# Kernel optimization log

Measured on AMD Instinct MI355X. Metric: run time of the kernel, lower is better.

Reference implementation:

```python
import jax, jax.numpy as jnp
import numpy as np

B, S, D, HU = 64, 512, 256, 1024
W_SCALE = 0.01  # flax nn.initializers.normal() default stddev


def setup_inputs() -> dict:
    key = jax.random.key(0)
    ks = jax.random.split(key, 13)
    inp = {
        "inputs": jax.random.normal(ks[0], (B, S, D), dtype=jnp.float32),
        "H0": jax.random.normal(ks[1], (B, HU), dtype=jnp.float32),
        "C0": jax.random.normal(ks[2], (B, HU), dtype=jnp.float32),
        "Wxi": jax.random.normal(ks[3], (D, HU), dtype=jnp.float32) * W_SCALE,
        "Whi": jax.random.normal(ks[4], (HU, HU), dtype=jnp.float32) * W_SCALE,
        "bi": jnp.zeros((HU,), dtype=jnp.float32),
        "Wxf": jax.random.normal(ks[5], (D, HU), dtype=jnp.float32) * W_SCALE,
        "Whf": jax.random.normal(ks[6], (HU, HU), dtype=jnp.float32) * W_SCALE,
        "bf": jnp.zeros((HU,), dtype=jnp.float32),
        "Wxo": jax.random.normal(ks[7], (D, HU), dtype=jnp.float32) * W_SCALE,
        "Who": jax.random.normal(ks[8], (HU, HU), dtype=jnp.float32) * W_SCALE,
        "bo": jnp.zeros((HU,), dtype=jnp.float32),
        "Wxc": jax.random.normal(ks[9], (D, HU), dtype=jnp.float32) * W_SCALE,
        "Whc": jax.random.normal(ks[10], (HU, HU), dtype=jnp.float32) * W_SCALE,
        "bc": jnp.zeros((HU,), dtype=jnp.float32),
        "Wd": jax.random.normal(ks[11], (HU, 1), dtype=jnp.float32) * W_SCALE,
        "bd": jnp.zeros((1,), dtype=jnp.float32),
    }
    return inp


def _lstm_forward(inputs, H0, C0, Wxi, Whi, bi, Wxf, Whf, bf,
                  Wxo, Who, bo, Wxc, Whc, bc, Wd, bd):
    Hn = H0.shape[1]
    # Pack the 4 gate projections so the input GEMM is done once for all timesteps.
    Wx = jnp.concatenate([Wxi, Wxf, Wxo, Wxc], axis=1)  # (D, 4H)
    Wh = jnp.concatenate([Whi, Whf, Who, Whc], axis=1)  # (H, 4H)
    b = jnp.concatenate([bi, bf, bo, bc])                # (4H,)
    xg = jnp.einsum('bsd,dk->bsk', inputs, Wx) + b       # (B, S, 4H)

    def step(carry, xg_t):
        H, C = carry
        g = xg_t + H @ Wh                                # (B, 4H)
        i = jax.nn.sigmoid(g[:, :Hn])
        f = jax.nn.sigmoid(g[:, Hn:2 * Hn])
        o = jax.nn.sigmoid(g[:, 2 * Hn:3 * Hn])
        c_tilde = jnp.tanh(g[:, 3 * Hn:])
        C = f * C + i * c_tilde
        H = o * jnp.tanh(C)
        return (H, C), H

    (Hf, Cf), Hs = jax.lax.scan(step, (H0, C0), jnp.swapaxes(xg, 0, 1))
    outputs = jnp.swapaxes(Hs, 0, 1)                     # (B, S, H)
    pred = outputs @ Wd + bd                             # (B, S, 1)
    return pred, (Hf, Cf)


def reference(inputs, H0, C0, Wxi, Whi, bi, Wxf, Whf, bf,
              Wxo, Who, bo, Wxc, Whc, bc, Wd, bd):
    return _lstm_forward(inputs, H0, C0, Wxi, Whi, bi, Wxf, Whf, bf,
                         Wxo, Who, bo, Wxc, Whc, bc, Wd, bd)
```

## Files before the change

### kernel.cpp

```cpp
#include <hip/hip_runtime.h>


#define NB   128
#define SEQ  512
#define BATCH 64
#define DIM  256
#define HU   1024
#define ROWU 1032

typedef unsigned short u16;
typedef unsigned int   u32;
typedef unsigned long long u64;
typedef __attribute__((ext_vector_type(8))) short  short8;
typedef __attribute__((ext_vector_type(4))) float  f32x4;

typedef const __attribute__((address_space(1))) void* gptr_t;
typedef __attribute__((address_space(3))) void*       lptr_t;

__device__ __forceinline__ u16 f2bf(float x) {
  u32 u = __float_as_uint(x);
  u32 r = (u + 0x7FFFu + ((u >> 16) & 1u)) >> 16;
  return (u16)r;
}
__device__ __forceinline__ float sigf(float x)  { return 1.0f / (1.0f + __expf(-x)); }
__device__ __forceinline__ float tanhfast(float x) { return 1.0f - 2.0f / (1.0f + __expf(2.0f * x)); }
__device__ __forceinline__ short8 cv8(uint4 v) {
  union { uint4 d; short8 s; } u; u.d = v; return u.s;
}


__global__ void k_prep(const float* __restrict__ H0, u16* __restrict__ Hbuf0,
                       u32* __restrict__ flags) {
  int i = blockIdx.x * 256 + threadIdx.x;
  if (i < 2048) flags[i] = 0u;
  Hbuf0[i] = f2bf(H0[i]);
}

__global__ void k_xconv(const float* __restrict__ in, u16* __restrict__ out) {
  int i = blockIdx.x * 256 + threadIdx.x;
  float4 v = ((const float4*)in)[i];
  ushort4 o;
  o.x = f2bf(v.x); o.y = f2bf(v.y); o.z = f2bf(v.z); o.w = f2bf(v.w);
  ((ushort4*)out)[i] = o;
}

__global__ void k_pack(const float* __restrict__ Wxi, const float* __restrict__ Whi,
                       const float* __restrict__ Wxf, const float* __restrict__ Whf,
                       const float* __restrict__ Wxo, const float* __restrict__ Who,
                       const float* __restrict__ Wxc, const float* __restrict__ Whc,
                       u16* __restrict__ Wpack) {
  int tid  = blockIdx.x * 256 + threadIdx.x;
  int lane = tid & 63;
  int kc   = (tid >> 6) % 40;
  int nt   = ((tid >> 6) / 40) & 7;
  int bj   = (tid >> 6) / 320;
  int c    = nt * 16 + (lane & 15);
  int gate = (c >> 3) & 3;
  int h    = bj * 32 + (c >> 5) * 8 + (c & 7);
  const float* Wx = (gate == 0) ? Wxi : (gate == 1) ? Wxf : (gate == 2) ? Wxo : Wxc;
  const float* Wh = (gate == 0) ? Whi : (gate == 1) ? Whf : (gate == 2) ? Who : Whc;
  int kbase = kc * 32 + ((lane >> 4) << 3);
  u16 tmp[8];
#pragma unroll
  for (int e = 0; e < 8; e++) {
    int k = kbase + e;
    float v = (k < DIM) ? Wx[k * HU + h] : Wh[(k - DIM) * HU + h];
    tmp[e] = f2bf(v);
  }
  *(uint4*)(Wpack + (size_t)tid * 8) = *(uint4*)tmp;
}

__global__ void k_predsum(const float* __restrict__ part, const float* __restrict__ bd,
                          float* __restrict__ pred) {
  int i = blockIdx.x * 256 + threadIdx.x;
  int b = i & 63, t = i >> 6;
  float s = bd[0];
  const float* p0 = part + (size_t)t * NB * 64 + b;
#pragma unroll 8
  for (int jj = 0; jj < NB; jj++) s += p0[jj * 64];
  pred[b * SEQ + t] = s;
}


struct MainParams {
  const u16* __restrict__ xbf;
  const u16* __restrict__ Wpack;
  u16* __restrict__ Hbuf;
  const float* __restrict__ C0;
  const float* __restrict__ Wd;
  const float* __restrict__ bi;
  const float* __restrict__ bfg;
  const float* __restrict__ bo;
  const float* __restrict__ bc;
  float* __restrict__ ppart;
  float* __restrict__ Hf;
  float* __restrict__ Cf;
  u32* __restrict__ flags;
};

__global__ __launch_bounds__(256, 1) void lstm_main(MainParams p) {
  __shared__ __align__(16) u16 Hsm[16 * ROWU];

  const int tid  = threadIdx.x;
  const int wv   = tid >> 6, lane = tid & 63;
  const int bj   = blockIdx.x >> 2, bb = blockIdx.x & 3;
  const int q    = lane >> 4;
  const int q8   = q * 8;
  const int m16  = lane & 15;
  const int hl   = lane & 7;
  const bool hiH = (lane & 8) != 0;

  const int hglob = bj * 32 + wv * 8 + hl;
  const int row0  = 16 * bb;

  short8 wx[8][2], wh[32][2];
  {
    const u16* wbase = p.Wpack + ((size_t)bj * 8 + 2 * wv) * (40 * 512) + lane * 8;
#pragma unroll
    for (int kc = 0; kc < 8; kc++)
#pragma unroll
      for (int ntl = 0; ntl < 2; ntl++)
        wx[kc][ntl] = *(const short8*)(wbase + ((size_t)ntl * 40 + kc) * 512);
#pragma unroll
    for (int kc = 0; kc < 32; kc++)
#pragma unroll
      for (int ntl = 0; ntl < 2; ntl++)
        wh[kc][ntl] = *(const short8*)(wbase + ((size_t)ntl * 40 + 8 + kc) * 512);
  }

  const float bI = p.bi[hglob],  bF = p.bfg[hglob];
  const float bO = p.bo[hglob],  bC = p.bc[hglob];
  const float wdv = p.Wd[hglob];
  float Cst[4], Hst[4];
#pragma unroll
  for (int r = 0; r < 4; r++) {
    Cst[r] = p.C0[(row0 + q * 4 + r) * HU + hglob];
    Hst[r] = 0.f;
  }

  const u16* Aw = Hsm + m16 * ROWU + q8;

  uint4 ax[8];
#pragma unroll
  for (int kc = 0; kc < 8; kc++)
    ax[kc] = *(const uint4*)(p.xbf + ((size_t)((row0 + m16) * SEQ + 0)) * DIM
                             + kc * 32 + q8);

#pragma unroll 1
  for (int t = 0; t < SEQ; t++) {
    const int rb = t & 1;
    const u16* Hr = p.Hbuf + (size_t)rb * (BATCH * HU);
    u16*       Hw = p.Hbuf + (size_t)(rb ^ 1) * (BATCH * HU);

#pragma unroll
    for (int i = 0; i < 8; i++) {
      int s = wv * 8 + i, row = s >> 1, half = s & 1;
      const u16* g = Hr + (size_t)(row0 + row) * HU + half * 512 + lane * 8;
      __builtin_amdgcn_global_load_lds((gptr_t)(const void*)g,
          (lptr_t)(void*)(Hsm + row * ROWU + half * 512), 16, 0, 17);
    }

    f32x4 acc[2][4];
#pragma unroll
    for (int ntl = 0; ntl < 2; ntl++)
#pragma unroll
      for (int c = 0; c < 4; c++) acc[ntl][c] = (f32x4){0.f, 0.f, 0.f, 0.f};
#pragma unroll
    for (int kc = 0; kc < 8; kc++) {
      short8 af = cv8(ax[kc]);
      acc[0][kc & 3] = __builtin_amdgcn_mfma_f32_16x16x32_bf16(af, wx[kc][0], acc[0][kc & 3], 0, 0, 0);
      acc[1][kc & 3] = __builtin_amdgcn_mfma_f32_16x16x32_bf16(af, wx[kc][1], acc[1][kc & 3], 0, 0, 0);
    }

    __syncthreads();

    {
      const int tn = (t + 1 < SEQ) ? t + 1 : t;
#pragma unroll
      for (int kc = 0; kc < 8; kc++)
        ax[kc] = *(const uint4*)(p.xbf + ((size_t)((row0 + m16) * SEQ + tn)) * DIM
                                 + kc * 32 + q8);
    }

#pragma unroll
    for (int kc = 0; kc < 32; kc++) {
      short8 af = *(const short8*)(Aw + kc * 32);
      acc[0][kc & 3] = __builtin_amdgcn_mfma_f32_16x16x32_bf16(af, wh[kc][0], acc[0][kc & 3], 0, 0, 0);
      acc[1][kc & 3] = __builtin_amdgcn_mfma_f32_16x16x32_bf16(af, wh[kc][1], acc[1][kc & 3], 0, 0, 0);
    }

    f32x4 g01 = (acc[0][0] + acc[0][1]) + (acc[0][2] + acc[0][3]);
    f32x4 g23 = (acc[1][0] + acc[1][1]) + (acc[1][2] + acc[1][3]);

    float pr[4];
#pragma unroll
    for (int r = 0; r < 4; r++) {
      float u0 = g01[r], u1 = g23[r];
      float v0 = __shfl_xor(u0, 8);
      float v1 = __shfl_xor(u1, 8);
      float gi = hiH ? v0 : u0, gf = hiH ? u0 : v0;
      float go = hiH ? v1 : u1, gc = hiH ? u1 : v1;
      float iv = sigf(gi + bI), fv = sigf(gf + bF);
      float ov = sigf(go + bO), ct = tanhfast(gc + bC);
      Cst[r] = fv * Cst[r] + iv * ct;
      Hst[r] = ov * tanhfast(Cst[r]);
      pr[r]  = Hst[r] * wdv;
    }

    if (!hiH) {
#pragma unroll
      for (int r = 0; r < 4; r++)
        __hip_atomic_store(Hw + (size_t)(row0 + q * 4 + r) * HU + hglob,
                           f2bf(Hst[r]), __ATOMIC_RELAXED, __HIP_MEMORY_SCOPE_AGENT);
    }

#pragma unroll
    for (int r = 0; r < 4; r++) {
      pr[r] += __shfl_xor(pr[r], 1);
      pr[r] += __shfl_xor(pr[r], 2);
      pr[r] += __shfl_xor(pr[r], 4);
    }
    if (m16 == 0) {
      float4 st = {pr[0], pr[1], pr[2], pr[3]};
      *(float4*)(p.ppart + (((size_t)t * 32 + bj) * 4 + wv) * 64 + row0 + q * 4) = st;
    }

    __syncthreads();
    if (tid == 0)
      __hip_atomic_store(p.flags + (bb * 32 + bj) * 16, (u32)(t + 1),
                         __ATOMIC_RELAXED, __HIP_MEMORY_SCOPE_AGENT);
    if (tid < 32) {
      const u32* f = p.flags + (bb * 32 + tid) * 16;
      while (__hip_atomic_load(f, __ATOMIC_RELAXED, __HIP_MEMORY_SCOPE_AGENT) < (u32)(t + 1))
        __builtin_amdgcn_s_sleep(1);
    }
    __syncthreads();
  }

  if (!hiH) {
#pragma unroll
    for (int r = 0; r < 4; r++) {
      int row = row0 + q * 4 + r;
      p.Hf[row * HU + hglob] = Hst[r];
      p.Cf[row * HU + hglob] = Cst[r];
    }
  }
}


extern "C" void kernel_launch(void* const* d_in, const int* in_sizes, int n_in,
                              void* d_out, int out_size, void* d_ws, size_t ws_size,
                              hipStream_t stream) {
  const float* inputs = (const float*)d_in[0];
  const float* H0  = (const float*)d_in[1];
  const float* C0  = (const float*)d_in[2];
  const float* Wxi = (const float*)d_in[3];
  const float* Whi = (const float*)d_in[4];
  const float* bi  = (const float*)d_in[5];
  const float* Wxf = (const float*)d_in[6];
  const float* Whf = (const float*)d_in[7];
  const float* bf_ = (const float*)d_in[8];
  const float* Wxo = (const float*)d_in[9];
  const float* Who = (const float*)d_in[10];
  const float* bo  = (const float*)d_in[11];
  const float* Wxc = (const float*)d_in[12];
  const float* Whc = (const float*)d_in[13];
  const float* bc  = (const float*)d_in[14];
  const float* Wd  = (const float*)d_in[15];
  const float* bd  = (const float*)d_in[16];

  char* ws = (char*)d_ws;
  u32*   flags = (u32*)ws;
  u16*   Wpack = (u16*)(ws + 8192);
  u16*   xbf   = (u16*)(ws + 8192 + 10485760);
  u16*   Hbuf  = (u16*)(ws + 8192 + 10485760 + 16777216);
  float* ppart = (float*)(ws + 8192 + 10485760 + 16777216 + 262144);

  float* pred = (float*)d_out;
  float* Hf   = pred + BATCH * SEQ;
  float* Cf   = Hf + BATCH * HU;

  k_prep<<<256, 256, 0, stream>>>(H0, Hbuf, flags);
  k_xconv<<<8192, 256, 0, stream>>>(inputs, xbf);
  k_pack<<<2560, 256, 0, stream>>>(Wxi, Whi, Wxf, Whf, Wxo, Who, Wxc, Whc, Wpack);

  MainParams prm{xbf, Wpack, Hbuf, C0, Wd, bi, bf_, bo, bc, ppart, Hf, Cf, flags};
  lstm_main<<<dim3(NB), dim3(256), 0, stream>>>(prm);

  k_predsum<<<128, 256, 0, stream>>>(ppart, bd, pred);
}
```

Measured before the change: 2.338 ms.

## Replace block barriers with per-wave flags and stream H directly from global

Drops the two __syncthreads-based block-level handshakes. Each wave now publishes its own progress flag after storing its slice of H, and all 64 lanes poll the 128 wave flags for their batch group before reading H. The recurrent A operand is read with relaxed atomic 64-bit global loads straight into registers, double-buffered across groups of four k-chunks, so the LDS staging copy goes away. The new H values are packed through a small LDS buffer so each wave writes contiguous 16-byte rows. This is meant to shorten the per-step critical path, at the cost of more flag polling traffic and correctness that depends on waitcnt ordering of the relaxed stores.

```diff
diff --git a/kernel.cpp b/kernel.cpp
--- a/kernel.cpp
+++ b/kernel.cpp
@@ -6,7 +6,6 @@
 #define BATCH 64
 #define DIM  256
 #define HU   1024
-#define ROWU 1032
 
 typedef unsigned short u16;
 typedef unsigned int   u32;
@@ -14,8 +13,8 @@
 typedef __attribute__((ext_vector_type(8))) short  short8;
 typedef __attribute__((ext_vector_type(4))) float  f32x4;
 
-typedef const __attribute__((address_space(1))) void* gptr_t;
-typedef __attribute__((address_space(3))) void*       lptr_t;
+#define AL_RLX(p)    __hip_atomic_load((p),  __ATOMIC_RELAXED, __HIP_MEMORY_SCOPE_AGENT)
+#define AS_RLX(p, v) __hip_atomic_store((p), (v), __ATOMIC_RELAXED, __HIP_MEMORY_SCOPE_AGENT)
 
 __device__ __forceinline__ u16 f2bf(float x) {
   u32 u = __float_as_uint(x);
@@ -27,12 +26,15 @@
 __device__ __forceinline__ short8 cv8(uint4 v) {
   union { uint4 d; short8 s; } u; u.d = v; return u.s;
 }
+__device__ __forceinline__ short8 mk8(u64 lo, u64 hi) {
+  union { u64 d[2]; short8 s; } u; u.d[0] = lo; u.d[1] = hi; return u.s;
+}
 
 
 __global__ void k_prep(const float* __restrict__ H0, u16* __restrict__ Hbuf0,
                        u32* __restrict__ flags) {
   int i = blockIdx.x * 256 + threadIdx.x;
-  if (i < 2048) flags[i] = 0u;
+  if (i < 8192) flags[i] = 0u;
   Hbuf0[i] = f2bf(H0[i]);
 }
 
@@ -99,7 +101,7 @@
 };
 
 __global__ __launch_bounds__(256, 1) void lstm_main(MainParams p) {
-  __shared__ __align__(16) u16 Hsm[16 * ROWU];
+  __shared__ u16 Hpub[4 * 128];
 
   const int tid  = threadIdx.x;
   const int wv   = tid >> 6, lane = tid & 63;
@@ -138,13 +140,14 @@
     Hst[r] = 0.f;
   }
 
-  const u16* Aw = Hsm + m16 * ROWU + q8;
-
   uint4 ax[8];
 #pragma unroll
   for (int kc = 0; kc < 8; kc++)
     ax[kc] = *(const uint4*)(p.xbf + ((size_t)((row0 + m16) * SEQ + 0)) * DIM
                              + kc * 32 + q8);
+
+  const u32* fbase = p.flags + (size_t)bb * 128 * 16;
+  u32* myflag = p.flags + ((size_t)(bb * 32 + bj) * 4 + wv) * 16;
 
 #pragma unroll 1
   for (int t = 0; t < SEQ; t++) {
@@ -152,12 +155,26 @@
     const u16* Hr = p.Hbuf + (size_t)rb * (BATCH * HU);
     u16*       Hw = p.Hbuf + (size_t)(rb ^ 1) * (BATCH * HU);
 
-#pragma unroll
-    for (int i = 0; i < 8; i++) {
-      int s = wv * 8 + i, row = s >> 1, half = s & 1;
-      const u16* g = Hr + (size_t)(row0 + row) * HU + half * 512 + lane * 8;
-      __builtin_amdgcn_global_load_lds((gptr_t)(const void*)g,
-          (lptr_t)(void*)(Hsm + row * ROWU + half * 512), 16, 0, 17);
+    {
+      const u32 tgt = (u32)t;
+      while (true) {
+        u32 a = AL_RLX(fbase + (size_t)lane * 16);
+        u32 b = AL_RLX(fbase + (size_t)(lane + 64) * 16);
+        if (__all((a >= tgt) && (b >= tgt))) break;
+      }
+    }
+
+    const u16* Arow = Hr + (size_t)(row0 + m16) * HU + q8;
+    u64 ah[2][4][2];
+#pragma unroll
+    for (int kcl = 0; kcl < 4; kcl++) {
+      const u64* hp = (const u64*)(Arow + (0 * 4 + kcl) * 32);
+      ah[0][kcl][0] = AL_RLX(hp); ah[0][kcl][1] = AL_RLX(hp + 1);
+    }
+#pragma unroll
+    for (int kcl = 0; kcl < 4; kcl++) {
+      const u64* hp = (const u64*)(Arow + (1 * 4 + kcl) * 32);
+      ah[1][kcl][0] = AL_RLX(hp); ah[1][kcl][1] = AL_RLX(hp + 1);
     }
 
     f32x4 acc[2][4];
@@ -172,21 +189,22 @@
       acc[1][kc & 3] = __builtin_amdgcn_mfma_f32_16x16x32_bf16(af, wx[kc][1], acc[1][kc & 3], 0, 0, 0);
     }
 
-    __syncthreads();
-
-    {
-      const int tn = (t + 1 < SEQ) ? t + 1 : t;
-#pragma unroll
-      for (int kc = 0; kc < 8; kc++)
-        ax[kc] = *(const uint4*)(p.xbf + ((size_t)((row0 + m16) * SEQ + tn)) * DIM
-                                 + kc * 32 + q8);
-    }
-
-#pragma unroll
-    for (int kc = 0; kc < 32; kc++) {
-      short8 af = *(const short8*)(Aw + kc * 32);
-      acc[0][kc & 3] = __builtin_amdgcn_mfma_f32_16x16x32_bf16(af, wh[kc][0], acc[0][kc & 3], 0, 0, 0);
-      acc[1][kc & 3] = __builtin_amdgcn_mfma_f32_16x16x32_bf16(af, wh[kc][1], acc[1][kc & 3], 0, 0, 0);
+#pragma unroll
+    for (int g = 0; g < 8; g++) {
+      const int fb = g & 1;
+#pragma unroll
+      for (int kcl = 0; kcl < 4; kcl++) {
+        short8 af = mk8(ah[fb][kcl][0], ah[fb][kcl][1]);
+        acc[0][kcl] = __builtin_amdgcn_mfma_f32_16x16x32_bf16(af, wh[g * 4 + kcl][0], acc[0][kcl], 0, 0, 0);
+        acc[1][kcl] = __builtin_amdgcn_mfma_f32_16x16x32_bf16(af, wh[g * 4 + kcl][1], acc[1][kcl], 0, 0, 0);
+      }
+      if (g < 6) {
+#pragma unroll
+        for (int kcl = 0; kcl < 4; kcl++) {
+          const u64* hp = (const u64*)(Arow + ((g + 2) * 4 + kcl) * 32);
+          ah[fb][kcl][0] = AL_RLX(hp); ah[fb][kcl][1] = AL_RLX(hp + 1);
+        }
+      }
     }
 
     f32x4 g01 = (acc[0][0] + acc[0][1]) + (acc[0][2] + acc[0][3]);
@@ -207,13 +225,6 @@
       pr[r]  = Hst[r] * wdv;
     }
 
-    if (!hiH) {
-#pragma unroll
-      for (int r = 0; r < 4; r++)
-        __hip_atomic_store(Hw + (size_t)(row0 + q * 4 + r) * HU + hglob,
-                           f2bf(Hst[r]), __ATOMIC_RELAXED, __HIP_MEMORY_SCOPE_AGENT);
-    }
-
 #pragma unroll
     for (int r = 0; r < 4; r++) {
       pr[r] += __shfl_xor(pr[r], 1);
@@ -225,16 +236,32 @@
       *(float4*)(p.ppart + (((size_t)t * 32 + bj) * 4 + wv) * 64 + row0 + q * 4) = st;
     }
 
-    __syncthreads();
-    if (tid == 0)
-      __hip_atomic_store(p.flags + (bb * 32 + bj) * 16, (u32)(t + 1),
-                         __ATOMIC_RELAXED, __HIP_MEMORY_SCOPE_AGENT);
-    if (tid < 32) {
-      const u32* f = p.flags + (bb * 32 + tid) * 16;
-      while (__hip_atomic_load(f, __ATOMIC_RELAXED, __HIP_MEMORY_SCOPE_AGENT) < (u32)(t + 1))
-        __builtin_amdgcn_s_sleep(1);
-    }
-    __syncthreads();
+    if (!hiH) {
+#pragma unroll
+      for (int r = 0; r < 4; r++)
+        Hpub[wv * 128 + (q * 4 + r) * 8 + hl] = f2bf(Hst[r]);
+    }
+    __builtin_amdgcn_s_waitcnt(0xC07F);
+    __builtin_amdgcn_wave_barrier();
+    if (lane < 16) {
+      const u64* src = (const u64*)(Hpub + wv * 128 + lane * 8);
+      u64 lo = src[0], hi = src[1];
+      u64* dst = (u64*)(Hw + (size_t)(row0 + lane) * HU + bj * 32 + wv * 8);
+      AS_RLX(dst, lo); AS_RLX(dst + 1, hi);
+    }
+    __builtin_amdgcn_sched_barrier(0);
+    __builtin_amdgcn_s_waitcnt(0x0F70);
+    __builtin_amdgcn_sched_barrier(0);
+    if (lane == 0) AS_RLX(myflag, (u32)(t + 1));
+    __builtin_amdgcn_sched_barrier(0);
+
+    {
+      const int tn = (t + 1 < SEQ) ? t + 1 : t;
+#pragma unroll
+      for (int kc = 0; kc < 8; kc++)
+        ax[kc] = *(const uint4*)(p.xbf + ((size_t)((row0 + m16) * SEQ + tn)) * DIM
+                                 + kc * 32 + q8);
+    }
   }
 
   if (!hiH) {
@@ -271,10 +298,10 @@
 
   char* ws = (char*)d_ws;
   u32*   flags = (u32*)ws;
-  u16*   Wpack = (u16*)(ws + 8192);
-  u16*   xbf   = (u16*)(ws + 8192 + 10485760);
-  u16*   Hbuf  = (u16*)(ws + 8192 + 10485760 + 16777216);
-  float* ppart = (float*)(ws + 8192 + 10485760 + 16777216 + 262144);
+  u16*   Wpack = (u16*)(ws + 32768);
+  u16*   xbf   = (u16*)(ws + 32768 + 10485760);
+  u16*   Hbuf  = (u16*)(ws + 32768 + 10485760 + 16777216);
+  float* ppart = (float*)(ws + 32768 + 10485760 + 16777216 + 262144);
 
   float* pred = (float*)d_out;
   float* Hf   = pred + BATCH * SEQ;
```

New measurement: 5.674 ms. 143% more time.

## Replace end-of-step block barriers with per-wave LDS counter and wave-wide flag polling

Applied to the files above, without the earlier changes.

Moves the cross-block flag wait to the start of each step, polled by a whole wave with __all, and double-buffers the shared H tile so the end-of-step __syncthreads pairs can be removed. Each wave stages its bf16 H outputs in LDS and writes them to global as 64-bit stores instead of scattered 16-bit atomic stores. Waves signal completion through a shared-memory atomic counter, and thread 0 publishes the block flag once all four waves have checked in. The goal is to cut barrier and fine-grained store overhead on the serial recurrence critical path. The cost is subtler memory-ordering reliance on raw s_waitcnt encodings and relaxed atomics, with a risk of visibility races.

```diff
diff --git a/kernel.cpp b/kernel.cpp
--- a/kernel.cpp
+++ b/kernel.cpp
@@ -16,6 +16,9 @@
 
 typedef const __attribute__((address_space(1))) void* gptr_t;
 typedef __attribute__((address_space(3))) void*       lptr_t;
+
+#define AL_RLX(p)    __hip_atomic_load((p),  __ATOMIC_RELAXED, __HIP_MEMORY_SCOPE_AGENT)
+#define AS_RLX(p, v) __hip_atomic_store((p), (v), __ATOMIC_RELAXED, __HIP_MEMORY_SCOPE_AGENT)
 
 __device__ __forceinline__ u16 f2bf(float x) {
   u32 u = __float_as_uint(x);
@@ -99,7 +102,9 @@
 };
 
 __global__ __launch_bounds__(256, 1) void lstm_main(MainParams p) {
-  __shared__ __align__(16) u16 Hsm[16 * ROWU];
+  __shared__ __align__(16) u16 Hsm[2][16 * ROWU];
+  __shared__ u16 Hpub[4 * 128];
+  __shared__ u32 cnt;
 
   const int tid  = threadIdx.x;
   const int wv   = tid >> 6, lane = tid & 63;
@@ -138,26 +143,40 @@
     Hst[r] = 0.f;
   }
 
-  const u16* Aw = Hsm + m16 * ROWU + q8;
-
   uint4 ax[8];
 #pragma unroll
   for (int kc = 0; kc < 8; kc++)
     ax[kc] = *(const uint4*)(p.xbf + ((size_t)((row0 + m16) * SEQ + 0)) * DIM
                              + kc * 32 + q8);
+
+  if (tid == 0) cnt = 0u;
+  __syncthreads();
+
+  const u32* fbase = p.flags + (size_t)bb * 32 * 16;
+  u32* myflag = p.flags + (size_t)(bb * 32 + bj) * 16;
 
 #pragma unroll 1
   for (int t = 0; t < SEQ; t++) {
     const int rb = t & 1;
     const u16* Hr = p.Hbuf + (size_t)rb * (BATCH * HU);
     u16*       Hw = p.Hbuf + (size_t)(rb ^ 1) * (BATCH * HU);
+    u16*       smb = &Hsm[t & 1][0];
+
+    {
+      const u32 tgt = (u32)t;
+      while (true) {
+        u32 a = AL_RLX(fbase + (size_t)(lane & 31) * 16);
+        if (__all((int)(a >= tgt))) break;
+        __builtin_amdgcn_s_sleep(1);
+      }
+    }
 
 #pragma unroll
     for (int i = 0; i < 8; i++) {
       int s = wv * 8 + i, row = s >> 1, half = s & 1;
       const u16* g = Hr + (size_t)(row0 + row) * HU + half * 512 + lane * 8;
       __builtin_amdgcn_global_load_lds((gptr_t)(const void*)g,
-          (lptr_t)(void*)(Hsm + row * ROWU + half * 512), 16, 0, 17);
+          (lptr_t)(void*)(smb + row * ROWU + half * 512), 16, 0, 17);
     }
 
     f32x4 acc[2][4];
@@ -171,9 +190,6 @@
       acc[0][kc & 3] = __builtin_amdgcn_mfma_f32_16x16x32_bf16(af, wx[kc][0], acc[0][kc & 3], 0, 0, 0);
       acc[1][kc & 3] = __builtin_amdgcn_mfma_f32_16x16x32_bf16(af, wx[kc][1], acc[1][kc & 3], 0, 0, 0);
     }
-
-    __syncthreads();
-
     {
       const int tn = (t + 1 < SEQ) ? t + 1 : t;
 #pragma unroll
@@ -182,9 +198,11 @@
                                  + kc * 32 + q8);
     }
 
+    __syncthreads();
+
 #pragma unroll
     for (int kc = 0; kc < 32; kc++) {
-      short8 af = *(const short8*)(Aw + kc * 32);
+      short8 af = *(const short8*)(smb + m16 * ROWU + kc * 32 + q8);
       acc[0][kc & 3] = __builtin_amdgcn_mfma_f32_16x16x32_bf16(af, wh[kc][0], acc[0][kc & 3], 0, 0, 0);
       acc[1][kc & 3] = __builtin_amdgcn_mfma_f32_16x16x32_bf16(af, wh[kc][1], acc[1][kc & 3], 0, 0, 0);
     }
@@ -207,13 +225,6 @@
       pr[r]  = Hst[r] * wdv;
     }
 
-    if (!hiH) {
-#pragma unroll
-      for (int r = 0; r < 4; r++)
-        __hip_atomic_store(Hw + (size_t)(row0 + q * 4 + r) * HU + hglob,
-                           f2bf(Hst[r]), __ATOMIC_RELAXED, __HIP_MEMORY_SCOPE_AGENT);
-    }
-
 #pragma unroll
     for (int r = 0; r < 4; r++) {
       pr[r] += __shfl_xor(pr[r], 1);
@@ -225,16 +236,29 @@
       *(float4*)(p.ppart + (((size_t)t * 32 + bj) * 4 + wv) * 64 + row0 + q * 4) = st;
     }
 
-    __syncthreads();
-    if (tid == 0)
-      __hip_atomic_store(p.flags + (bb * 32 + bj) * 16, (u32)(t + 1),
-                         __ATOMIC_RELAXED, __HIP_MEMORY_SCOPE_AGENT);
-    if (tid < 32) {
-      const u32* f = p.flags + (bb * 32 + tid) * 16;
-      while (__hip_atomic_load(f, __ATOMIC_RELAXED, __HIP_MEMORY_SCOPE_AGENT) < (u32)(t + 1))
-        __builtin_amdgcn_s_sleep(1);
-    }
-    __syncthreads();
+    if (!hiH) {
+#pragma unroll
+      for (int r = 0; r < 4; r++)
+        Hpub[wv * 128 + (q * 4 + r) * 8 + hl] = f2bf(Hst[r]);
+    }
+    __builtin_amdgcn_s_waitcnt(0xC07F);
+    __builtin_amdgcn_wave_barrier();
+    if (lane < 16) {
+      const u64* src = (const u64*)(Hpub + wv * 128 + lane * 8);
+      u64 lo = src[0], hi = src[1];
+      u64* dst = (u64*)(Hw + (size_t)(row0 + lane) * HU + bj * 32 + wv * 8);
+      AS_RLX(dst, lo); AS_RLX(dst + 1, hi);
+    }
+    __builtin_amdgcn_sched_barrier(0);
+    __builtin_amdgcn_s_waitcnt(0x0F70);
+    __builtin_amdgcn_sched_barrier(0);
+    if (lane == 0)
+      __hip_atomic_fetch_add(&cnt, 1u, __ATOMIC_RELAXED, __HIP_MEMORY_SCOPE_WORKGROUP);
+    if (tid == 0) {
+      while (__hip_atomic_load(&cnt, __ATOMIC_RELAXED, __HIP_MEMORY_SCOPE_WORKGROUP)
+             < 4u * (u32)(t + 1)) {}
+      AS_RLX(myflag, (u32)(t + 1));
+    }
   }
 
   if (!hiH) {
```

After: 2.836 ms. 21.3% more time.
